# Kernel tuning notes

Hardware: AMD Instinct MI355X
Metric: run time of the kernel (lower is better)

The kernel has to match this reference:

```python
import jax, jax.numpy as jnp
import numpy as np

N_NODES = 100000
N_EDGES = 1600000
D = 128
N_LAYERS = 3


def setup_inputs() -> dict:
    key = jax.random.key(0)
    ks = jax.random.split(key, 6)
    x = jax.random.normal(ks[0], (N_NODES, D), dtype=jnp.float32)
    edge_index = jax.random.randint(ks[1], (2, N_EDGES), 0, N_NODES, dtype=jnp.int64)
    # GIN MLP params per layer: Linear(D,D) -> ReLU -> Linear(D,D)
    W1 = jax.random.normal(ks[2], (N_LAYERS, D, D), dtype=jnp.float32) * 0.05
    b1 = jnp.zeros((N_LAYERS, D), dtype=jnp.float32)
    W2 = jax.random.normal(ks[3], (N_LAYERS, D, D), dtype=jnp.float32) * 0.05
    b2 = jnp.zeros((N_LAYERS, D), dtype=jnp.float32)
    return {"x": x, "edge_index": edge_index, "W1": W1, "b1": b1, "W2": W2, "b2": b2}


def reference(x, edge_index, W1, b1, W2, b2):
    # MultiscaleEncoder with conv='GIN', conv_dropout=0 (dropout skipped).
    # GINConv (eps=0): out = MLP(x + sum_{src->dst} x[src]), aggregated at dst.
    src, dst = edge_index[0], edge_index[1]
    n = x.shape[0]
    outs = []
    for l in range(W1.shape[0]):
        agg = jax.ops.segment_sum(x[src], dst, num_segments=n)  # [N, D]
        h = x + agg  # (1 + eps) * x + agg with eps = 0
        h = jax.nn.relu(h @ W1[l] + b1[l])
        h = h @ W2[l] + b2[l]
        x = jax.nn.relu(h)  # per-layer ReLU in MultiscaleEncoder.forward
        outs.append(x)
    return jnp.stack(outs)  # [n_layers, N, D]
```

## Files before the change

kernel.cpp:

```cpp
#include <hip/hip_runtime.h>

#define D 128

typedef __attribute__((ext_vector_type(8))) short bf16x8;
typedef __attribute__((ext_vector_type(4))) float f32x4;

__device__ inline unsigned short f2b(float f) {
    union { float f; unsigned int u; } v; v.f = f;
    unsigned int u = v.u;
    u += 0x7fffu + ((u >> 16) & 1u);
    return (unsigned short)(u >> 16);
}
__device__ inline float bl(unsigned int u) { union { unsigned int u; float f; } c; c.u = u << 16; return c.f; }
__device__ inline float bh(unsigned int u) { union { unsigned int u; float f; } c; c.u = u & 0xffff0000u; return c.f; }

__global__ void detect_dtype(const int* __restrict__ ei, int E, int* __restrict__ flag) {
    if (blockIdx.x == 0 && threadIdx.x == 0) {
        int z = 0;
        int nprobe = (E > 32) ? 32 : E;
        for (int i = 0; i < nprobe; i++) z |= ei[2 * i + 1];
        flag[0] = (z == 0) ? 1 : 0;
    }
}

__global__ void count_deg_part(const int* __restrict__ ei, int E, int n,
                               const int* __restrict__ flag, int* __restrict__ deg) {
    int grp = blockIdx.x & 7;
    int per = n >> 3;
    int r0 = grp * per;
    int r1 = (grp == 7) ? n : r0 + per;
    int m = flag[0];
    int tpg = (gridDim.x >> 3) * blockDim.x;
    int idx = (blockIdx.x >> 3) * blockDim.x + threadIdx.x;
    for (int i = idx; i < E; i += tpg) {
        int d = m ? ei[2 * (E + i)] : ei[E + i];
        if (d >= r0 && d < r1) atomicAdd(&deg[d], 1);
    }
}

__global__ void fill_csr_part(const int* __restrict__ ei, int E, int n,
                              const int* __restrict__ flag, const int* __restrict__ offsets,
                              int* __restrict__ cursor, int* __restrict__ csr) {
    int grp = blockIdx.x & 7;
    int per = n >> 3;
    int r0 = grp * per;
    int r1 = (grp == 7) ? n : r0 + per;
    int m = flag[0];
    int tpg = (gridDim.x >> 3) * blockDim.x;
    int idx = (blockIdx.x >> 3) * blockDim.x + threadIdx.x;
    for (int i = idx; i < E; i += tpg) {
        int d = m ? ei[2 * (E + i)] : ei[E + i];
        if (d >= r0 && d < r1) {
            int s = m ? ei[2 * i] : ei[i];
            int pos = offsets[d] + atomicAdd(&cursor[d], 1);
            csr[pos] = s;
        }
    }
}

__global__ void partial_sums(const int* __restrict__ deg, int* __restrict__ blksum, int n) {
    __shared__ int s[256];
    int i = blockIdx.x * 256 + threadIdx.x;
    s[threadIdx.x] = (i < n) ? deg[i] : 0;
    __syncthreads();
    for (int off = 128; off; off >>= 1) {
        if (threadIdx.x < off) s[threadIdx.x] += s[threadIdx.x + off];
        __syncthreads();
    }
    if (threadIdx.x == 0) blksum[blockIdx.x] = s[0];
}

__global__ void scan_blksum(int* __restrict__ blksum, int nb) {
    __shared__ int s[1024];
    __shared__ int base_s;
    int tid = threadIdx.x;
    if (tid == 0) base_s = 0;
    __syncthreads();
    for (int start = 0; start < nb; start += 1024) {
        int idx = start + tid;
        int v = (idx < nb) ? blksum[idx] : 0;
        s[tid] = v;
        __syncthreads();
        for (int off = 1; off < 1024; off <<= 1) {
            int t = (tid >= off) ? s[tid - off] : 0;
            __syncthreads();
            s[tid] += t;
            __syncthreads();
        }
        int total = s[1023];
        if (idx < nb) blksum[idx] = base_s + s[tid] - v;
        __syncthreads();
        if (tid == 0) base_s += total;
        __syncthreads();
    }
}

__global__ void scan_fill(const int* __restrict__ deg, const int* __restrict__ blksum,
                          int* __restrict__ offsets, int n) {
    __shared__ int s[256];
    int tid = threadIdx.x;
    int i = blockIdx.x * 256 + tid;
    int v = (i < n) ? deg[i] : 0;
    s[tid] = v;
    __syncthreads();
    for (int off = 1; off < 256; off <<= 1) {
        int t = (tid >= off) ? s[tid - off] : 0;
        __syncthreads();
        s[tid] += t;
        __syncthreads();
    }
    if (i < n) offsets[i + 1] = blksum[blockIdx.x] + s[tid];
    if (i == 0) offsets[0] = 0;
}

__global__ void conv_w(const float* __restrict__ W1, const float* __restrict__ W2,
                       unsigned short* __restrict__ Wt, int L) {
    int i = blockIdx.x * blockDim.x + threadIdx.x;
    int total = L * 2 * D * D;
    if (i >= total) return;
    int l = i / (2 * D * D);
    int rem = i - l * 2 * D * D;
    int which = rem / (D * D);
    int idx = rem - which * D * D;
    int c = idx >> 7, k = idx & 127;
    const float* W = which ? W2 : W1;
    Wt[i] = f2b(W[(size_t)l * D * D + k * D + c]);
}

__global__ void conv_x(const float* __restrict__ x, unsigned short* __restrict__ xb, int total4) {
    int i = blockIdx.x * blockDim.x + threadIdx.x;
    if (i >= total4) return;
    float4 v = ((const float4*)x)[i];
    uint2 o;
    o.x = (unsigned int)f2b(v.x) | ((unsigned int)f2b(v.y) << 16);
    o.y = (unsigned int)f2b(v.z) | ((unsigned int)f2b(v.w) << 16);
    ((uint2*)xb)[i] = o;
}

__global__ void agg_bf16(const unsigned short* __restrict__ xb, const int* __restrict__ csr,
                         const int* __restrict__ offs, unsigned short* __restrict__ A, int n) {
    int node = blockIdx.x * (blockDim.x >> 6) + (threadIdx.x >> 6);
    if (node >= n) return;
    int lane = threadIdx.x & 63;
    int half = lane >> 5, l32 = lane & 31;
    const uint2* xv = (const uint2*)xb;

    float a0 = 0.f, a1 = 0.f, a2 = 0.f, a3 = 0.f;
    if (half == 0) {
        uint2 sv = xv[(size_t)node * 32 + l32];
        a0 += bl(sv.x); a1 += bh(sv.x); a2 += bl(sv.y); a3 += bh(sv.y);
    }
    int beg = offs[node], end = offs[node + 1];
    int i = beg + half;
    for (; i + 6 < end; i += 8) {
        int s0 = csr[i], s1 = csr[i + 2], s2 = csr[i + 4], s3 = csr[i + 6];
        uint2 v0 = xv[(size_t)s0 * 32 + l32];
        uint2 v1 = xv[(size_t)s1 * 32 + l32];
        uint2 v2 = xv[(size_t)s2 * 32 + l32];
        uint2 v3 = xv[(size_t)s3 * 32 + l32];
        a0 += bl(v0.x); a1 += bh(v0.x); a2 += bl(v0.y); a3 += bh(v0.y);
        a0 += bl(v1.x); a1 += bh(v1.x); a2 += bl(v1.y); a3 += bh(v1.y);
        a0 += bl(v2.x); a1 += bh(v2.x); a2 += bl(v2.y); a3 += bh(v2.y);
        a0 += bl(v3.x); a1 += bh(v3.x); a2 += bl(v3.y); a3 += bh(v3.y);
    }
    for (; i < end; i += 2) {
        int s0 = csr[i];
        uint2 v0 = xv[(size_t)s0 * 32 + l32];
        a0 += bl(v0.x); a1 += bh(v0.x); a2 += bl(v0.y); a3 += bh(v0.y);
    }
    a0 += __shfl_xor(a0, 32);
    a1 += __shfl_xor(a1, 32);
    a2 += __shfl_xor(a2, 32);
    a3 += __shfl_xor(a3, 32);
    if (half == 0) {
        uint2 o;
        o.x = (unsigned int)f2b(a0) | ((unsigned int)f2b(a1) << 16);
        o.y = (unsigned int)f2b(a2) | ((unsigned int)f2b(a3) << 16);
        ((uint2*)A)[(size_t)node * 32 + l32] = o;
    }
}

__global__ void agg_f32(const float* __restrict__ x, const int* __restrict__ csr,
                        const int* __restrict__ offsets, unsigned short* __restrict__ A, int n) {
    int node = blockIdx.x * (blockDim.x >> 6) + (threadIdx.x >> 6);
    if (node >= n) return;
    int d2 = threadIdx.x & 63;
    const float2* xr = (const float2*)(x + (size_t)node * D);
    float2 acc = xr[d2];
    int beg = offsets[node], end = offsets[node + 1];
    for (int i = beg; i < end; i++) {
        int s = csr[i];
        float2 v = ((const float2*)(x + (size_t)s * D))[d2];
        acc.x += v.x; acc.y += v.y;
    }
    unsigned int pk = (unsigned int)f2b(acc.x) | ((unsigned int)f2b(acc.y) << 16);
    ((unsigned int*)(A + (size_t)node * D))[d2] = pk;
}

__global__ __launch_bounds__(256) void mlp_fused(
    const unsigned short* __restrict__ Ain,
    const unsigned short* __restrict__ Wt1,
    const unsigned short* __restrict__ Wt2,
    const float* __restrict__ b1, const float* __restrict__ b2,
    int n, float* __restrict__ outF, unsigned short* __restrict__ outXB) {

    __shared__ unsigned char Hs[128 * 128 * 2];

    int wave = threadIdx.x >> 6;
    int lane = threadIdx.x & 63;
    int l16 = lane & 15, g = lane >> 4;
    int rowbase = blockIdx.x * 128 + wave * 32;

    f32x4 acc[2][8];
    #pragma unroll
    for (int rf = 0; rf < 2; rf++)
        #pragma unroll
        for (int cf = 0; cf < 8; cf++)
            acc[rf][cf] = (f32x4){0.f, 0.f, 0.f, 0.f};

    #pragma unroll
    for (int ks = 0; ks < 4; ks++) {
        int k0 = ks * 32 + g * 8;
        bf16x8 a[2];
        #pragma unroll
        for (int rf = 0; rf < 2; rf++) {
            int row = rowbase + rf * 16 + l16;
            if (row >= n) row = n - 1;
            a[rf] = *((const bf16x8*)(Ain + (size_t)row * D + k0));
        }
        #pragma unroll
        for (int cf = 0; cf < 8; cf++) {
            int col = cf * 16 + l16;
            bf16x8 b = *((const bf16x8*)(Wt1 + col * D + k0));
            acc[0][cf] = __builtin_amdgcn_mfma_f32_16x16x32_bf16(a[0], b, acc[0][cf], 0, 0, 0);
            acc[1][cf] = __builtin_amdgcn_mfma_f32_16x16x32_bf16(a[1], b, acc[1][cf], 0, 0, 0);
        }
    }

    #pragma unroll
    for (int cf = 0; cf < 8; cf++) {
        int col = cf * 16 + l16;
        float bv = b1[col];
        #pragma unroll
        for (int rf = 0; rf < 2; rf++) {
            #pragma unroll
            for (int r = 0; r < 4; r++) {
                int rl = wave * 32 + rf * 16 + g * 4 + r;
                float v = acc[rf][cf][r] + bv;
                v = (v < 0.f) ? 0.f : v;
                int byte = (rl * 256 + col * 2) ^ ((rl & 7) << 4);
                *(unsigned short*)(Hs + byte) = f2b(v);
            }
        }
    }
    __syncthreads();

    f32x4 acc2[2][8];
    #pragma unroll
    for (int rf = 0; rf < 2; rf++)
        #pragma unroll
        for (int cf = 0; cf < 8; cf++)
            acc2[rf][cf] = (f32x4){0.f, 0.f, 0.f, 0.f};

    #pragma unroll
    for (int ks = 0; ks < 4; ks++) {
        int k0 = ks * 32 + g * 8;
        bf16x8 a[2];
        #pragma unroll
        for (int rf = 0; rf < 2; rf++) {
            int rl = wave * 32 + rf * 16 + l16;
            int byte = (rl * 256 + k0 * 2) ^ ((rl & 7) << 4);
            a[rf] = *(const bf16x8*)(Hs + byte);
        }
        #pragma unroll
        for (int cf = 0; cf < 8; cf++) {
            int col = cf * 16 + l16;
            bf16x8 b = *((const bf16x8*)(Wt2 + col * D + k0));
            acc2[0][cf] = __builtin_amdgcn_mfma_f32_16x16x32_bf16(a[0], b, acc2[0][cf], 0, 0, 0);
            acc2[1][cf] = __builtin_amdgcn_mfma_f32_16x16x32_bf16(a[1], b, acc2[1][cf], 0, 0, 0);
        }
    }

    #pragma unroll
    for (int cf = 0; cf < 8; cf++) {
        int col = cf * 16 + l16;
        float bv = b2[col];
        #pragma unroll
        for (int rf = 0; rf < 2; rf++) {
            #pragma unroll
            for (int r = 0; r < 4; r++) {
                int row = rowbase + rf * 16 + g * 4 + r;
                if (row < n) {
                    float v = acc2[rf][cf][r] + bv;
                    v = (v < 0.f) ? 0.f : v;
                    outF[(size_t)row * D + col] = v;
                    if (outXB) outXB[(size_t)row * D + col] = f2b(v);
                }
            }
        }
    }
}

extern "C" void kernel_launch(void* const* d_in, const int* in_sizes, int n_in,
                              void* d_out, int out_size, void* d_ws, size_t ws_size,
                              hipStream_t stream) {
    const float* x  = (const float*)d_in[0];
    const int*   ei = (const int*)d_in[1];
    const float* W1 = (const float*)d_in[2];
    const float* b1 = (const float*)d_in[3];
    const float* W2 = (const float*)d_in[4];
    const float* b2 = (const float*)d_in[5];
    float* out = (float*)d_out;

    int N = in_sizes[0] / D;
    int E = in_sizes[1] / 2;
    int L = in_sizes[3] / D;
    int NB = (N + 255) / 256;

    auto alignup = [](size_t v) { return (v + 255) & ~(size_t)255; };
    size_t sz_flag = 256;
    size_t sz_deg  = alignup((size_t)N * 4);
    size_t sz_offs = alignup((size_t)(N + 1) * 4);
    size_t sz_cur  = alignup((size_t)N * 4);
    size_t sz_blk  = alignup((size_t)NB * 4);
    size_t sz_csr  = alignup((size_t)E * 4);
    size_t sz_wt   = alignup((size_t)L * 2 * D * D * 2);
    size_t sz_mat  = alignup((size_t)N * D * 2);
    size_t base = sz_flag + sz_deg + sz_offs + sz_cur + sz_blk + sz_csr + sz_wt;
    bool useBf16 = (base + 2 * sz_mat) <= ws_size;

    char* p = (char*)d_ws;
    int* flag    = (int*)p;            p += sz_flag;
    int* deg     = (int*)p;            p += sz_deg;
    int* offs    = (int*)p;            p += sz_offs;
    int* cursor  = (int*)p;            p += sz_cur;
    int* blksum  = (int*)p;            p += sz_blk;
    int* csr     = (int*)p;            p += sz_csr;
    unsigned short* Wt = (unsigned short*)p; p += sz_wt;
    unsigned short* A  = (unsigned short*)p; p += sz_mat;
    unsigned short* XB = (unsigned short*)p;

    hipMemsetAsync(deg, 0, (size_t)N * 4, stream);
    hipMemsetAsync(cursor, 0, (size_t)N * 4, stream);

    detect_dtype<<<1, 64, 0, stream>>>(ei, E, flag);
    count_deg_part<<<2048, 256, 0, stream>>>(ei, E, N, flag, deg);
    partial_sums<<<NB, 256, 0, stream>>>(deg, blksum, N);
    scan_blksum<<<1, 1024, 0, stream>>>(blksum, NB);
    scan_fill<<<NB, 256, 0, stream>>>(deg, blksum, offs, N);
    fill_csr_part<<<2048, 256, 0, stream>>>(ei, E, N, flag, offs, cursor, csr);
    conv_w<<<(L * 2 * D * D + 255) / 256, 256, 0, stream>>>(W1, W2, Wt, L);
    if (useBf16)
        conv_x<<<(N * D / 4 + 255) / 256, 256, 0, stream>>>(x, XB, N * D / 4);

    for (int l = 0; l < L; l++) {
        if (useBf16) {
            agg_bf16<<<(N + 3) / 4, 256, 0, stream>>>(XB, csr, offs, A, N);
        } else {
            const float* xin = (l == 0) ? x : out + (size_t)(l - 1) * N * D;
            agg_f32<<<(N + 3) / 4, 256, 0, stream>>>(xin, csr, offs, A, N);
        }
        unsigned short* nextXB = (useBf16 && l + 1 < L) ? XB : nullptr;
        mlp_fused<<<(N + 127) / 128, 256, 0, stream>>>(
            A, Wt + (size_t)l * 2 * D * D, Wt + (size_t)l * 2 * D * D + D * D,
            b1 + (size_t)l * D, b2 + (size_t)l * D, N,
            out + (size_t)l * N * D, nextXB);
    }
}
```

Before: 578.4 us.

## Fuse neighbor aggregation into GIN MLP kernel via shared-memory staging

The separate aggregation kernel is removed. Each MLP block now gathers and sums neighbor features for its own 128 rows directly into swizzled shared memory, then runs the MFMA MLP from that tile. This drops the global write and re-read of the aggregated matrix and one launch per layer, and double-buffers the bf16 feature array between layers. The CSR fill also takes its cursor from the scan output, which removes the cursor memset and the offsets lookup. The trade-off is that each wave processes one node at a time serially (32 per wave), which cuts gather parallelism and latency hiding compared with the old kernel's four nodes per block with split halves.

Result: slower. 786.4 us (+36.0%).

```diff
diff --git a/kernel.cpp b/kernel.cpp
--- a/kernel.cpp
+++ b/kernel.cpp
@@ -39,8 +39,8 @@
 }
 
 __global__ void fill_csr_part(const int* __restrict__ ei, int E, int n,
-                              const int* __restrict__ flag, const int* __restrict__ offsets,
-                              int* __restrict__ cursor, int* __restrict__ csr) {
+                              const int* __restrict__ flag,
+                              int* __restrict__ cur, int* __restrict__ csr) {
     int grp = blockIdx.x & 7;
     int per = n >> 3;
     int r0 = grp * per;
@@ -52,7 +52,7 @@
         int d = m ? ei[2 * (E + i)] : ei[E + i];
         if (d >= r0 && d < r1) {
             int s = m ? ei[2 * i] : ei[i];
-            int pos = offsets[d] + atomicAdd(&cursor[d], 1);
+            int pos = atomicAdd(&cur[d], 1);
             csr[pos] = s;
         }
     }
@@ -96,7 +96,7 @@
 }
 
 __global__ void scan_fill(const int* __restrict__ deg, const int* __restrict__ blksum,
-                          int* __restrict__ offsets, int n) {
+                          int* __restrict__ offsets, int* __restrict__ cur, int n) {
     __shared__ int s[256];
     int tid = threadIdx.x;
     int i = blockIdx.x * 256 + tid;
@@ -109,7 +109,11 @@
         s[tid] += t;
         __syncthreads();
     }
-    if (i < n) offsets[i + 1] = blksum[blockIdx.x] + s[tid];
+    if (i < n) {
+        int inc = blksum[blockIdx.x] + s[tid];
+        offsets[i + 1] = inc;
+        cur[i] = inc - v;
+    }
     if (i == 0) offsets[0] = 0;
 }
 
@@ -137,80 +141,78 @@
     ((uint2*)xb)[i] = o;
 }
 
-__global__ void agg_bf16(const unsigned short* __restrict__ xb, const int* __restrict__ csr,
-                         const int* __restrict__ offs, unsigned short* __restrict__ A, int n) {
-    int node = blockIdx.x * (blockDim.x >> 6) + (threadIdx.x >> 6);
-    if (node >= n) return;
-    int lane = threadIdx.x & 63;
-    int half = lane >> 5, l32 = lane & 31;
-    const uint2* xv = (const uint2*)xb;
-
-    float a0 = 0.f, a1 = 0.f, a2 = 0.f, a3 = 0.f;
-    if (half == 0) {
-        uint2 sv = xv[(size_t)node * 32 + l32];
-        a0 += bl(sv.x); a1 += bh(sv.x); a2 += bl(sv.y); a3 += bh(sv.y);
-    }
-    int beg = offs[node], end = offs[node + 1];
-    int i = beg + half;
-    for (; i + 6 < end; i += 8) {
-        int s0 = csr[i], s1 = csr[i + 2], s2 = csr[i + 4], s3 = csr[i + 6];
-        uint2 v0 = xv[(size_t)s0 * 32 + l32];
-        uint2 v1 = xv[(size_t)s1 * 32 + l32];
-        uint2 v2 = xv[(size_t)s2 * 32 + l32];
-        uint2 v3 = xv[(size_t)s3 * 32 + l32];
-        a0 += bl(v0.x); a1 += bh(v0.x); a2 += bl(v0.y); a3 += bh(v0.y);
-        a0 += bl(v1.x); a1 += bh(v1.x); a2 += bl(v1.y); a3 += bh(v1.y);
-        a0 += bl(v2.x); a1 += bh(v2.x); a2 += bl(v2.y); a3 += bh(v2.y);
-        a0 += bl(v3.x); a1 += bh(v3.x); a2 += bl(v3.y); a3 += bh(v3.y);
-    }
-    for (; i < end; i += 2) {
-        int s0 = csr[i];
-        uint2 v0 = xv[(size_t)s0 * 32 + l32];
-        a0 += bl(v0.x); a1 += bh(v0.x); a2 += bl(v0.y); a3 += bh(v0.y);
-    }
-    a0 += __shfl_xor(a0, 32);
-    a1 += __shfl_xor(a1, 32);
-    a2 += __shfl_xor(a2, 32);
-    a3 += __shfl_xor(a3, 32);
-    if (half == 0) {
-        uint2 o;
-        o.x = (unsigned int)f2b(a0) | ((unsigned int)f2b(a1) << 16);
-        o.y = (unsigned int)f2b(a2) | ((unsigned int)f2b(a3) << 16);
-        ((uint2*)A)[(size_t)node * 32 + l32] = o;
-    }
-}
-
-__global__ void agg_f32(const float* __restrict__ x, const int* __restrict__ csr,
-                        const int* __restrict__ offsets, unsigned short* __restrict__ A, int n) {
-    int node = blockIdx.x * (blockDim.x >> 6) + (threadIdx.x >> 6);
-    if (node >= n) return;
-    int d2 = threadIdx.x & 63;
-    const float2* xr = (const float2*)(x + (size_t)node * D);
-    float2 acc = xr[d2];
-    int beg = offsets[node], end = offsets[node + 1];
-    for (int i = beg; i < end; i++) {
-        int s = csr[i];
-        float2 v = ((const float2*)(x + (size_t)s * D))[d2];
-        acc.x += v.x; acc.y += v.y;
-    }
-    unsigned int pk = (unsigned int)f2b(acc.x) | ((unsigned int)f2b(acc.y) << 16);
-    ((unsigned int*)(A + (size_t)node * D))[d2] = pk;
-}
-
-__global__ __launch_bounds__(256) void mlp_fused(
-    const unsigned short* __restrict__ Ain,
+__global__ __launch_bounds__(256) void gin_mlp(
+    const unsigned short* __restrict__ xb,
+    const float* __restrict__ xf,
+    const int* __restrict__ csr, const int* __restrict__ offs,
     const unsigned short* __restrict__ Wt1,
     const unsigned short* __restrict__ Wt2,
     const float* __restrict__ b1, const float* __restrict__ b2,
     int n, float* __restrict__ outF, unsigned short* __restrict__ outXB) {
 
-    __shared__ unsigned char Hs[128 * 128 * 2];
+    __shared__ unsigned char Hs[128 * 256];
 
     int wave = threadIdx.x >> 6;
     int lane = threadIdx.x & 63;
     int l16 = lane & 15, g = lane >> 4;
     int rowbase = blockIdx.x * 128 + wave * 32;
 
+    const unsigned int* xv = (const unsigned int*)xb;
+    const float2* xr = (const float2*)xf;
+    for (int j = 0; j < 32; j++) {
+        int nd = rowbase + j;
+        float a0 = 0.f, a1 = 0.f;
+        if (nd < n) {
+            int ns = __builtin_amdgcn_readfirstlane(nd);
+            int beg = offs[ns], end = offs[ns + 1];
+            if (xb) {
+                unsigned int v = xv[(size_t)ns * 64 + lane];
+                a0 = bl(v); a1 = bh(v);
+                int p = beg;
+                for (; p + 8 <= end; p += 8) {
+                    int s0 = csr[p],     s1 = csr[p + 1], s2 = csr[p + 2], s3 = csr[p + 3];
+                    int s4 = csr[p + 4], s5 = csr[p + 5], s6 = csr[p + 6], s7 = csr[p + 7];
+                    unsigned int v0 = xv[(size_t)s0 * 64 + lane];
+                    unsigned int v1 = xv[(size_t)s1 * 64 + lane];
+                    unsigned int v2 = xv[(size_t)s2 * 64 + lane];
+                    unsigned int v3 = xv[(size_t)s3 * 64 + lane];
+                    unsigned int v4 = xv[(size_t)s4 * 64 + lane];
+                    unsigned int v5 = xv[(size_t)s5 * 64 + lane];
+                    unsigned int v6 = xv[(size_t)s6 * 64 + lane];
+                    unsigned int v7 = xv[(size_t)s7 * 64 + lane];
+                    a0 += bl(v0); a1 += bh(v0); a0 += bl(v1); a1 += bh(v1);
+                    a0 += bl(v2); a1 += bh(v2); a0 += bl(v3); a1 += bh(v3);
+                    a0 += bl(v4); a1 += bh(v4); a0 += bl(v5); a1 += bh(v5);
+                    a0 += bl(v6); a1 += bh(v6); a0 += bl(v7); a1 += bh(v7);
+                }
+                for (; p < end; p++) {
+                    unsigned int v0 = xv[(size_t)csr[p] * 64 + lane];
+                    a0 += bl(v0); a1 += bh(v0);
+                }
+            } else {
+                float2 sv = xr[(size_t)ns * 64 + lane];
+                a0 = sv.x; a1 = sv.y;
+                int p = beg;
+                for (; p + 4 <= end; p += 4) {
+                    int s0 = csr[p], s1 = csr[p + 1], s2 = csr[p + 2], s3 = csr[p + 3];
+                    float2 v0 = xr[(size_t)s0 * 64 + lane];
+                    float2 v1 = xr[(size_t)s1 * 64 + lane];
+                    float2 v2 = xr[(size_t)s2 * 64 + lane];
+                    float2 v3 = xr[(size_t)s3 * 64 + lane];
+                    a0 += v0.x + v1.x + v2.x + v3.x;
+                    a1 += v0.y + v1.y + v2.y + v3.y;
+                }
+                for (; p < end; p++) {
+                    float2 v0 = xr[(size_t)csr[p] * 64 + lane];
+                    a0 += v0.x; a1 += v0.y;
+                }
+            }
+        }
+        int rl = wave * 32 + j;
+        int byte = (rl * 256 + lane * 4) ^ ((rl & 7) << 4);
+        *(unsigned int*)(Hs + byte) = (unsigned int)f2b(a0) | ((unsigned int)f2b(a1) << 16);
+    }
+
     f32x4 acc[2][8];
     #pragma unroll
     for (int rf = 0; rf < 2; rf++)
@@ -224,9 +226,9 @@
         bf16x8 a[2];
         #pragma unroll
         for (int rf = 0; rf < 2; rf++) {
-            int row = rowbase + rf * 16 + l16;
-            if (row >= n) row = n - 1;
-            a[rf] = *((const bf16x8*)(Ain + (size_t)row * D + k0));
+            int rl = wave * 32 + rf * 16 + l16;
+            int byte = (rl * 256 + k0 * 2) ^ ((rl & 7) << 4);
+            a[rf] = *(const bf16x8*)(Hs + byte);
         }
         #pragma unroll
         for (int cf = 0; cf < 8; cf++) {
@@ -236,6 +238,7 @@
             acc[1][cf] = __builtin_amdgcn_mfma_f32_16x16x32_bf16(a[1], b, acc[1][cf], 0, 0, 0);
         }
     }
+    __syncthreads();
 
     #pragma unroll
     for (int cf = 0; cf < 8; cf++) {
@@ -333,36 +336,34 @@
     int* flag    = (int*)p;            p += sz_flag;
     int* deg     = (int*)p;            p += sz_deg;
     int* offs    = (int*)p;            p += sz_offs;
-    int* cursor  = (int*)p;            p += sz_cur;
+    int* cur     = (int*)p;            p += sz_cur;
     int* blksum  = (int*)p;            p += sz_blk;
     int* csr     = (int*)p;            p += sz_csr;
-    unsigned short* Wt = (unsigned short*)p; p += sz_wt;
-    unsigned short* A  = (unsigned short*)p; p += sz_mat;
-    unsigned short* XB = (unsigned short*)p;
+    unsigned short* Wt  = (unsigned short*)p; p += sz_wt;
+    unsigned short* XB0 = (unsigned short*)p; p += sz_mat;
+    unsigned short* XB1 = (unsigned short*)p;
 
     hipMemsetAsync(deg, 0, (size_t)N * 4, stream);
-    hipMemsetAsync(cursor, 0, (size_t)N * 4, stream);
 
     detect_dtype<<<1, 64, 0, stream>>>(ei, E, flag);
     count_deg_part<<<2048, 256, 0, stream>>>(ei, E, N, flag, deg);
     partial_sums<<<NB, 256, 0, stream>>>(deg, blksum, N);
     scan_blksum<<<1, 1024, 0, stream>>>(blksum, NB);
-    scan_fill<<<NB, 256, 0, stream>>>(deg, blksum, offs, N);
-    fill_csr_part<<<2048, 256, 0, stream>>>(ei, E, N, flag, offs, cursor, csr);
+    scan_fill<<<NB, 256, 0, stream>>>(deg, blksum, offs, cur, N);
+    fill_csr_part<<<2048, 256, 0, stream>>>(ei, E, N, flag, cur, csr);
     conv_w<<<(L * 2 * D * D + 255) / 256, 256, 0, stream>>>(W1, W2, Wt, L);
     if (useBf16)
-        conv_x<<<(N * D / 4 + 255) / 256, 256, 0, stream>>>(x, XB, N * D / 4);
+        conv_x<<<(N * D / 4 + 255) / 256, 256, 0, stream>>>(x, XB0, N * D / 4);
 
     for (int l = 0; l < L; l++) {
-        if (useBf16) {
-            agg_bf16<<<(N + 3) / 4, 256, 0, stream>>>(XB, csr, offs, A, N);
-        } else {
-            const float* xin = (l == 0) ? x : out + (size_t)(l - 1) * N * D;
-            agg_f32<<<(N + 3) / 4, 256, 0, stream>>>(xin, csr, offs, A, N);
-        }
-        unsigned short* nextXB = (useBf16 && l + 1 < L) ? XB : nullptr;
-        mlp_fused<<<(N + 127) / 128, 256, 0, stream>>>(
-            A, Wt + (size_t)l * 2 * D * D, Wt + (size_t)l * 2 * D * D + D * D,
+        unsigned short* XBin  = (l & 1) ? XB1 : XB0;
+        unsigned short* XBout = (l & 1) ? XB0 : XB1;
+        const unsigned short* xbin = useBf16 ? XBin : nullptr;
+        const float* xfin = (l == 0) ? x : out + (size_t)(l - 1) * N * D;
+        unsigned short* nextXB = (useBf16 && l + 1 < L) ? XBout : nullptr;
+        gin_mlp<<<(N + 127) / 128, 256, 0, stream>>>(
+            xbin, xfin, csr, offs,
+            Wt + (size_t)l * 2 * D * D, Wt + (size_t)l * 2 * D * D + D * D,
             b1 + (size_t)l * D, b2 + (size_t)l * D, N,
             out + (size_t)l * N * D, nextXB);
     }
```
